# Kernel tuning notes

Hardware: AMD Instinct MI355X
Metric: run time of the kernel (lower is better)

## Reference

```python
import jax, jax.numpy as jnp
import numpy as np

B, T, I, H, O = 128, 500, 512, 1024, 11
BETA, THRESH, GAMMA, SPARSITY = 0.9, 1.0, 0.5, 0.05

@jax.custom_vjp
def spike(x):
    return (x > 0).astype(x.dtype)

def _spike_fwd(x):
    return (x > 0).astype(x.dtype), x

def _spike_bwd(x, g):
    # surrogate gradient: gamma / (1 + |x|)^2
    return (g * GAMMA / jnp.square(1.0 + jnp.abs(x)),)

spike.defvjp(_spike_fwd, _spike_bwd)


def setup_inputs() -> dict:
    key = jax.random.key(0)
    k0, k1, k2, k3, k4 = jax.random.split(key, 5)
    x = jax.random.normal(k0, (B, T, I), jnp.float32)
    # xavier-uniform-like init for W_in / W_out, orthogonal-ish (scaled normal) for W_rec
    lim_in = (6.0 / (I + H)) ** 0.5
    lim_out = (6.0 / (H + O)) ** 0.5
    W_in = jax.random.uniform(k1, (I, H), jnp.float32, -lim_in, lim_in)
    W_rec = jax.random.normal(k2, (H, H), jnp.float32) / jnp.sqrt(jnp.float32(H))
    W_out = jax.random.uniform(k3, (H, O), jnp.float32, -lim_out, lim_out)
    # fixed sparse connectivity mask: Bernoulli(sparsity), no self-connections
    mask = (jax.random.uniform(k4, (H, H)) < SPARSITY).astype(jnp.float32)
    mask = mask * (1.0 - jnp.eye(H, dtype=jnp.float32))
    W_rec = W_rec * mask  # reset_parameters() applies mask at init when mask is not learnable
    h_bias = jnp.zeros((H,), jnp.float32)
    b_out = jnp.zeros((O,), jnp.float32)
    return {"x": x, "W_in": W_in, "W_rec": W_rec, "W_out": W_out,
            "h_bias": h_bias, "b_out": b_out, "mask": mask}


def reference(x, W_in, W_rec, W_out, h_bias, b_out, mask):
    W_eff = W_rec * mask                                   # masked recurrent weights [H,H]
    drive = jnp.einsum('bti,ih->bth', x, W_in) + h_bias    # per-step input drive [B,T,H]
    drive_t = jnp.swapaxes(drive, 0, 1)                    # [T,B,H]

    def step(carry, d_t):
        v, s = carry
        v = BETA * v + d_t + s @ W_eff                     # LIF membrane update
        s_new = spike(v - THRESH)                          # surrogate threshold spike
        v = v - jax.lax.stop_gradient(s_new) * THRESH      # subtract reset (detached)
        out_t = s_new @ W_out + b_out                      # per-step readout [B,O]
        return (v, s_new), out_t

    init = (jnp.zeros((x.shape[0], W_eff.shape[0]), x.dtype),
            jnp.zeros((x.shape[0], W_eff.shape[0]), x.dtype))
    _, outs = jax.lax.scan(step, init, drive_t)            # outs: [T,B,O]
    return jnp.mean(outs, axis=0)                          # 'rate' readout -> [B,O]
```

## Files before the change

### kernel.cpp

```cpp
#include <hip/hip_runtime.h>
#include <cstdint>
#include <cstddef>

#define B_ 128
#define T_ 500
#define I_ 512
#define H_ 1024
#define O_ 11
#define BETA 0.9f
#define THRESH 1.0f
#define K2_ 1536

typedef __attribute__((ext_vector_type(4))) float f32x4;
typedef __attribute__((ext_vector_type(8))) short bf16x8;
typedef __attribute__((ext_vector_type(4))) unsigned int u32x4;

__device__ __forceinline__ unsigned short bf16_rne(float f) {
  unsigned int u = __float_as_uint(f);
  unsigned int r = u + 0x7FFFu + ((u >> 16) & 1u);
  return (unsigned short)(r >> 16);
}
__device__ __forceinline__ float bf16_to_f(unsigned short h) {
  return __uint_as_float(((unsigned int)h) << 16);
}

__global__ void k_csr(const float* __restrict__ W_rec, const float* __restrict__ mask,
                      unsigned int* __restrict__ csr, unsigned int* __restrict__ rowhi) {
  int r = blockIdx.x * 4 + (threadIdx.x >> 6);
  if (r > 1024) return;
  int lane = threadIdx.x & 63;
  unsigned cnt = 0;
  if (r < 1024) {
    const float* mrow = mask + (size_t)r * H_;
    const float* wrow = W_rec + (size_t)r * H_;
    for (int c = 0; c < 16; ++c) {
      float m = mrow[c * 64 + lane];
      bool nz = (m != 0.f);
      unsigned long long bb = __ballot(nz);
      unsigned pos = cnt + (unsigned)__popcll(bb & ((1ull << lane) - 1ull));
      if (nz) {
        float w = wrow[c * 64 + lane] * m;
        int wi = __float2int_rn(w * 8388608.f);
        wi = wi > 2097151 ? 2097151 : (wi < -2097151 ? -2097151 : wi);
        if (pos < 128u) csr[((size_t)r << 7) + pos] = (((unsigned)wi) << 10) | (unsigned)(c * 64 + lane);
      }
      cnt += (unsigned)__popcll(bb);
    }
  }
  for (unsigned p = (cnt > 128u ? 128u : cnt) + (unsigned)lane; p < 128u; p += 64u)
    csr[((size_t)r << 7) + p] = (p & 63u);
  if (lane == 0) rowhi[r] = (cnt > 64u) ? 1u : 0u;
}

__global__ void k_build_wt(const float* __restrict__ W_in, unsigned short* __restrict__ Wt) {
  int n = blockIdx.y;
  int k2 = blockIdx.x * 256 + threadIdx.x;
  int i = k2 / 3;
  int c = k2 - 3 * i;
  float w = W_in[i * H_ + n];
  unsigned short hi = bf16_rne(w);
  unsigned short v = (c == 2) ? bf16_rne(w - bf16_to_f(hi)) : hi;
  Wt[(size_t)n * K2_ + k2] = v;
}

__global__ void k_build_xs(const float* __restrict__ x, unsigned short* __restrict__ xs,
                           int t0, int Tc) {
  int id = blockIdx.x * 256 + threadIdx.x;
  int rr = id >> 6;
  int oct = id & 63;
  int b = rr / Tc, tt = rr % Tc;
  const float4 v0 = *(const float4*)&x[((size_t)(b * T_ + t0 + tt)) * I_ + oct * 8];
  const float4 v1 = *(const float4*)&x[((size_t)(b * T_ + t0 + tt)) * I_ + oct * 8 + 4];
  alignas(16) unsigned short o[24];
  float vv[8] = {v0.x, v0.y, v0.z, v0.w, v1.x, v1.y, v1.z, v1.w};
#pragma unroll
  for (int j = 0; j < 8; ++j) {
    unsigned short hi = bf16_rne(vv[j]);
    unsigned short lo = bf16_rne(vv[j] - bf16_to_f(hi));
    o[3 * j + 0] = hi; o[3 * j + 1] = lo; o[3 * j + 2] = hi;
  }
  unsigned short* dst = xs + (size_t)rr * K2_ + oct * 24;
  *(u32x4*)(dst + 0) = *(u32x4*)(o + 0);
  *(u32x4*)(dst + 8) = *(u32x4*)(o + 8);
  *(u32x4*)(dst + 16) = *(u32x4*)(o + 16);
}

#define LDA 72
__global__ __launch_bounds__(512, 1) void k_gemm(const unsigned short* __restrict__ xs,
                                                 const unsigned short* __restrict__ Wt,
                                                 float* __restrict__ drive) {
  __shared__ __align__(16) unsigned short As[128 * LDA];
  __shared__ __align__(16) unsigned short Bs[256 * LDA];
  int mt = blockIdx.x, nt = blockIdx.y;
  int tid = threadIdx.x;
  int lane = tid & 63, w = tid >> 6;
  int wr = w >> 2, wc = w & 3;
  f32x4 acc[4][4] = {};
  int arow = tid >> 2, aq = tid & 3;
  int brow = tid >> 1, bh = tid & 1;
  const unsigned short* xsrow = xs + (size_t)(mt * 128 + arow) * K2_ + aq * 16;
  const unsigned short* wtrow = Wt + (size_t)(nt * 256 + brow) * K2_ + bh * 32;
  for (int kt = 0; kt < K2_ / 64; ++kt) {
    u32x4 a0 = *(const u32x4*)(xsrow + kt * 64);
    u32x4 a1 = *(const u32x4*)(xsrow + kt * 64 + 8);
    u32x4 b0 = *(const u32x4*)(wtrow + kt * 64);
    u32x4 b1 = *(const u32x4*)(wtrow + kt * 64 + 8);
    u32x4 b2 = *(const u32x4*)(wtrow + kt * 64 + 16);
    u32x4 b3 = *(const u32x4*)(wtrow + kt * 64 + 24);
    __syncthreads();
    *(u32x4*)&As[arow * LDA + aq * 16] = a0;
    *(u32x4*)&As[arow * LDA + aq * 16 + 8] = a1;
    *(u32x4*)&Bs[brow * LDA + bh * 32] = b0;
    *(u32x4*)&Bs[brow * LDA + bh * 32 + 8] = b1;
    *(u32x4*)&Bs[brow * LDA + bh * 32 + 16] = b2;
    *(u32x4*)&Bs[brow * LDA + bh * 32 + 24] = b3;
    __syncthreads();
#pragma unroll
    for (int kk = 0; kk < 2; ++kk) {
      bf16x8 af[4], bf[4];
#pragma unroll
      for (int mi = 0; mi < 4; ++mi)
        af[mi] = *(const bf16x8*)&As[(wr * 64 + mi * 16 + (lane & 15)) * LDA + kk * 32 + (lane >> 4) * 8];
#pragma unroll
      for (int ni = 0; ni < 4; ++ni)
        bf[ni] = *(const bf16x8*)&Bs[(wc * 64 + ni * 16 + (lane & 15)) * LDA + kk * 32 + (lane >> 4) * 8];
#pragma unroll
      for (int mi = 0; mi < 4; ++mi)
#pragma unroll
        for (int ni = 0; ni < 4; ++ni)
          acc[mi][ni] = __builtin_amdgcn_mfma_f32_16x16x32_bf16(af[mi], bf[ni], acc[mi][ni], 0, 0, 0);
    }
  }
  int r0 = (lane >> 4) * 4, c0 = lane & 15;
#pragma unroll
  for (int mi = 0; mi < 4; ++mi) {
    int rowb = mt * 128 + wr * 64 + mi * 16 + r0;
#pragma unroll
    for (int ni = 0; ni < 4; ++ni) {
      int col = nt * 256 + wc * 64 + ni * 16 + c0;
#pragma unroll
      for (int r = 0; r < 4; ++r)
        drive[(size_t)(rowb + r) * H_ + col] = acc[mi][ni][r];
    }
  }
}

__device__ __forceinline__ void step_one(
    float dcur, int cur, int tid, int lane, unsigned wvu, unsigned myhi, float bias,
    const unsigned int* __restrict__ csr, int* accL, unsigned int* listL, unsigned int* fcL,
    float& v, float& s, float& cnt) {
  unsigned F = (unsigned)__builtin_amdgcn_readfirstlane((int)fcL[cur]);
  unsigned lo = (F * wvu) >> 4;
  unsigned hi = (F * (wvu + 1u)) >> 4;
  for (unsigned i0 = lo; i0 < hi; i0 += 8u) {
    unsigned idx = i0 + ((unsigned)lane & 7u);
    unsigned packed = listL[idx < hi ? idx : (hi - 1u)];
#define EDECL(n) unsigned e##n = (i0 + n##u < hi) ? (unsigned)__builtin_amdgcn_readlane((int)packed, n) : 1024u; \
                 unsigned ea##n = 0u, eb##n = 0u;
    EDECL(0) EDECL(1) EDECL(2) EDECL(3) EDECL(4) EDECL(5) EDECL(6) EDECL(7)
#undef EDECL
#define ELOAD(n) if (e##n != 1024u) { \
      const unsigned int* rp = csr + ((size_t)(e##n & 1023u) << 7); \
      ea##n = rp[lane]; \
      if (e##n & 4096u) eb##n = rp[64 + lane]; }
    ELOAD(0) ELOAD(1) ELOAD(2) ELOAD(3) ELOAD(4) ELOAD(5) ELOAD(6) ELOAD(7)
#undef ELOAD
#define EATOM(n) if (e##n != 1024u) { \
      atomicAdd(&accL[ea##n & 1023u], ((int)ea##n) >> 10); \
      if (e##n & 4096u) atomicAdd(&accL[eb##n & 1023u], ((int)eb##n) >> 10); }
    EATOM(0) EATOM(1) EATOM(2) EATOM(3) EATOM(4) EATOM(5) EATOM(6) EATOM(7)
#undef EATOM
  }
  __syncthreads();
  int ri = accL[tid];
  accL[tid] = 0;
  v = BETA * v + (dcur + bias) + (float)ri * 1.1920929e-7f;
  bool f = v > THRESH;
  v -= f ? THRESH : 0.f;
  cnt += f ? 1.f : 0.f;
  s = f ? 1.f : 0.f;
  unsigned long long bb = __ballot(f);
  unsigned n = (unsigned)__popcll(bb);
  unsigned pos = (unsigned)__popcll(bb & ((1ull << lane) - 1ull));
  unsigned wb = 0;
  if (lane == 0) wb = atomicAdd(&fcL[cur ^ 1], n);
  wb = (unsigned)__builtin_amdgcn_readfirstlane((int)wb);
  if (f) listL[wb + pos] = (unsigned)tid | myhi;
  if (tid == 0) fcL[cur] = 0;
  __syncthreads();
}

__global__ __launch_bounds__(1024, 1) void k_rsnn(
    const float* __restrict__ drive, const unsigned int* __restrict__ csr,
    const unsigned int* __restrict__ rowhi,
    const float* __restrict__ h_bias, const float* __restrict__ W_out,
    const float* __restrict__ b_out,
    float* __restrict__ state_v, float* __restrict__ state_s, float* __restrict__ state_c,
    float* __restrict__ out, int t0, int Tc, int last) {
  __shared__ int accL[H_];
  __shared__ unsigned int listL[H_];
  __shared__ unsigned int fcL[2];
  __shared__ float red[H_];
  __shared__ float part[352];
  int tid = threadIdx.x;
  int b = blockIdx.x;
  int lane = tid & 63;
  unsigned wvu = (unsigned)__builtin_amdgcn_readfirstlane(tid >> 6);
  float bias = h_bias[tid];
  unsigned myhi = rowhi[tid] << 12;
  float v, s, cnt;
  if (t0 == 0) { v = 0.f; s = 0.f; cnt = 0.f; }
  else { v = state_v[b * H_ + tid]; s = state_s[b * H_ + tid]; cnt = state_c[b * H_ + tid]; }
  accL[tid] = 0;
  if (tid < 2) fcL[tid] = 0;
  __syncthreads();
  {
    bool f0 = s > 0.f;
    unsigned long long bb = __ballot(f0);
    unsigned n = (unsigned)__popcll(bb);
    unsigned pos = (unsigned)__popcll(bb & ((1ull << lane) - 1ull));
    unsigned wb = 0;
    if (lane == 0) wb = atomicAdd(&fcL[0], n);
    wb = (unsigned)__builtin_amdgcn_readfirstlane((int)wb);
    if (f0) listL[wb + pos] = (unsigned)tid | myhi;
  }
  __syncthreads();
  const float* dptr = drive + (size_t)b * Tc * H_ + tid;
  for (int t8 = 0; t8 < Tc; t8 += 8) {
    float dd0 = (t8 + 0 < Tc) ? dptr[(size_t)(t8 + 0) * H_] : 0.f;
    float dd1 = (t8 + 1 < Tc) ? dptr[(size_t)(t8 + 1) * H_] : 0.f;
    float dd2 = (t8 + 2 < Tc) ? dptr[(size_t)(t8 + 2) * H_] : 0.f;
    float dd3 = (t8 + 3 < Tc) ? dptr[(size_t)(t8 + 3) * H_] : 0.f;
    float dd4 = (t8 + 4 < Tc) ? dptr[(size_t)(t8 + 4) * H_] : 0.f;
    float dd5 = (t8 + 5 < Tc) ? dptr[(size_t)(t8 + 5) * H_] : 0.f;
    float dd6 = (t8 + 6 < Tc) ? dptr[(size_t)(t8 + 6) * H_] : 0.f;
    float dd7 = (t8 + 7 < Tc) ? dptr[(size_t)(t8 + 7) * H_] : 0.f;
#define STEP(s_) if (t8 + s_ < Tc) \
    step_one(dd##s_, (s_ & 1), tid, lane, wvu, myhi, bias, csr, accL, listL, fcL, v, s, cnt);
    STEP(0) STEP(1) STEP(2) STEP(3) STEP(4) STEP(5) STEP(6) STEP(7)
#undef STEP
  }
  if (!last) {
    state_v[b * H_ + tid] = v; state_s[b * H_ + tid] = s; state_c[b * H_ + tid] = cnt;
  } else {
    red[tid] = cnt;
    __syncthreads();
    if (tid < 352) {
      int o = tid >> 5, seg = tid & 31;
      float p = 0.f;
      for (int j = 0; j < 32; ++j) {
        int hh = seg * 32 + j;
        p += red[hh] * W_out[hh * O_ + o];
      }
      part[tid] = p;
    }
    __syncthreads();
    if (tid < O_) {
      float sum = 0.f;
      for (int g = 0; g < 32; ++g) sum += part[(tid << 5) + g];
      out[b * O_ + tid] = b_out[tid] + sum * (1.0f / (float)T_);
    }
  }
}

extern "C" void kernel_launch(void* const* d_in, const int* in_sizes, int n_in,
                              void* d_out, int out_size, void* d_ws, size_t ws_size,
                              hipStream_t stream) {
  (void)in_sizes; (void)n_in; (void)out_size;
  const float* x = (const float*)d_in[0];
  const float* W_in = (const float*)d_in[1];
  const float* W_rec = (const float*)d_in[2];
  const float* W_out = (const float*)d_in[3];
  const float* h_bias = (const float*)d_in[4];
  const float* b_out = (const float*)d_in[5];
  const float* mask = (const float*)d_in[6];
  float* out = (float*)d_out;

  char* ws = (char*)d_ws;
  size_t off = 0;
  auto alloc = [&](size_t bytes) {
    void* p = ws + off;
    off = (off + bytes + 255) & ~(size_t)255;
    return p;
  };
  unsigned short* Wt = (unsigned short*)alloc((size_t)H_ * K2_ * 2);
  unsigned int* csr = (unsigned int*)alloc((size_t)(H_ + 1) * 128 * 4);
  unsigned int* rowhi = (unsigned int*)alloc((size_t)(H_ + 1) * 4);
  float* st_v = (float*)alloc((size_t)B_ * H_ * 4);
  float* st_s = (float*)alloc((size_t)B_ * H_ * 4);
  float* st_c = (float*)alloc((size_t)B_ * H_ * 4);
  size_t fixed = off;

  size_t per_t = (size_t)128 * K2_ * 2 + (size_t)128 * 1024 * 4;
  int Tc = 1;
  if (ws_size > fixed + per_t) Tc = (int)((ws_size - fixed) / per_t);
  if (Tc > T_) Tc = T_;
  if (Tc < 1) Tc = 1;
  unsigned short* xs = (unsigned short*)alloc((size_t)128 * Tc * K2_ * 2);
  float* drive = (float*)alloc((size_t)128 * Tc * 1024 * 4);

  k_csr<<<dim3(257), dim3(256), 0, stream>>>(W_rec, mask, csr, rowhi);
  k_build_wt<<<dim3(6, 1024), dim3(256), 0, stream>>>(W_in, Wt);

  for (int t0 = 0; t0 < T_; t0 += Tc) {
    int tc = (Tc < T_ - t0) ? Tc : (T_ - t0);
    k_build_xs<<<dim3(32 * tc), dim3(256), 0, stream>>>(x, xs, t0, tc);
    k_gemm<<<dim3(tc, 4), dim3(512), 0, stream>>>(xs, Wt, drive);
    k_rsnn<<<dim3(128), dim3(1024), 0, stream>>>(drive, csr, rowhi, h_bias, W_out, b_out,
                                                 st_v, st_s, st_c, out, t0, tc,
                                                 (t0 + tc >= T_) ? 1 : 0);
  }
}
```

Baseline: 1.048 ms.

## Fuse x bf16 split into GEMM A-tile load and reorder K layout

Drops the separate k_build_xs kernel and its bf16x3 staging buffer. The GEMM now reads fp32 x directly and converts each A tile to hi or lo bf16 inside the load loop. K2 is reorganised from interleaved triples into three contiguous 512-wide segments (hi, lo, hi), and W_in is built to match. The GEMM grid is also swizzled so groups of 8 m-tiles share the same n-tile for better L2 reuse. This removes a full write and read of the expanded x array, but x is now reread three times and converted in the GEMM load path, which adds ALU work there.

```diff
diff --git a/kernel.cpp b/kernel.cpp
--- a/kernel.cpp
+++ b/kernel.cpp
@@ -27,25 +27,22 @@
 __global__ void k_csr(const float* __restrict__ W_rec, const float* __restrict__ mask,
                       unsigned int* __restrict__ csr, unsigned int* __restrict__ rowhi) {
   int r = blockIdx.x * 4 + (threadIdx.x >> 6);
-  if (r > 1024) return;
   int lane = threadIdx.x & 63;
   unsigned cnt = 0;
-  if (r < 1024) {
-    const float* mrow = mask + (size_t)r * H_;
-    const float* wrow = W_rec + (size_t)r * H_;
-    for (int c = 0; c < 16; ++c) {
-      float m = mrow[c * 64 + lane];
-      bool nz = (m != 0.f);
-      unsigned long long bb = __ballot(nz);
-      unsigned pos = cnt + (unsigned)__popcll(bb & ((1ull << lane) - 1ull));
-      if (nz) {
-        float w = wrow[c * 64 + lane] * m;
-        int wi = __float2int_rn(w * 8388608.f);
-        wi = wi > 2097151 ? 2097151 : (wi < -2097151 ? -2097151 : wi);
-        if (pos < 128u) csr[((size_t)r << 7) + pos] = (((unsigned)wi) << 10) | (unsigned)(c * 64 + lane);
-      }
-      cnt += (unsigned)__popcll(bb);
-    }
+  const float* mrow = mask + (size_t)r * H_;
+  const float* wrow = W_rec + (size_t)r * H_;
+  for (int c = 0; c < 16; ++c) {
+    float m = mrow[c * 64 + lane];
+    bool nz = (m != 0.f);
+    unsigned long long bb = __ballot(nz);
+    unsigned pos = cnt + (unsigned)__popcll(bb & ((1ull << lane) - 1ull));
+    if (nz) {
+      float w = wrow[c * 64 + lane] * m;
+      int wi = __float2int_rn(w * 8388608.f);
+      wi = wi > 2097151 ? 2097151 : (wi < -2097151 ? -2097151 : wi);
+      if (pos < 128u) csr[((size_t)r << 7) + pos] = (((unsigned)wi) << 10) | (unsigned)(c * 64 + lane);
+    }
+    cnt += (unsigned)__popcll(bb);
   }
   for (unsigned p = (cnt > 128u ? 128u : cnt) + (unsigned)lane; p < 128u; p += 64u)
     csr[((size_t)r << 7) + p] = (p & 63u);
@@ -55,61 +52,58 @@
 __global__ void k_build_wt(const float* __restrict__ W_in, unsigned short* __restrict__ Wt) {
   int n = blockIdx.y;
   int k2 = blockIdx.x * 256 + threadIdx.x;
-  int i = k2 / 3;
-  int c = k2 - 3 * i;
+  int i = k2 & 511;
+  int c = k2 >> 9;
   float w = W_in[i * H_ + n];
   unsigned short hi = bf16_rne(w);
   unsigned short v = (c == 2) ? bf16_rne(w - bf16_to_f(hi)) : hi;
   Wt[(size_t)n * K2_ + k2] = v;
 }
 
-__global__ void k_build_xs(const float* __restrict__ x, unsigned short* __restrict__ xs,
-                           int t0, int Tc) {
-  int id = blockIdx.x * 256 + threadIdx.x;
-  int rr = id >> 6;
-  int oct = id & 63;
-  int b = rr / Tc, tt = rr % Tc;
-  const float4 v0 = *(const float4*)&x[((size_t)(b * T_ + t0 + tt)) * I_ + oct * 8];
-  const float4 v1 = *(const float4*)&x[((size_t)(b * T_ + t0 + tt)) * I_ + oct * 8 + 4];
-  alignas(16) unsigned short o[24];
-  float vv[8] = {v0.x, v0.y, v0.z, v0.w, v1.x, v1.y, v1.z, v1.w};
-#pragma unroll
-  for (int j = 0; j < 8; ++j) {
-    unsigned short hi = bf16_rne(vv[j]);
-    unsigned short lo = bf16_rne(vv[j] - bf16_to_f(hi));
-    o[3 * j + 0] = hi; o[3 * j + 1] = lo; o[3 * j + 2] = hi;
-  }
-  unsigned short* dst = xs + (size_t)rr * K2_ + oct * 24;
-  *(u32x4*)(dst + 0) = *(u32x4*)(o + 0);
-  *(u32x4*)(dst + 8) = *(u32x4*)(o + 8);
-  *(u32x4*)(dst + 16) = *(u32x4*)(o + 16);
-}
-
 #define LDA 72
-__global__ __launch_bounds__(512, 1) void k_gemm(const unsigned short* __restrict__ xs,
+__global__ __launch_bounds__(512, 1) void k_gemm(const float* __restrict__ x,
                                                  const unsigned short* __restrict__ Wt,
-                                                 float* __restrict__ drive) {
+                                                 float* __restrict__ drive,
+                                                 int t0, int Tc) {
   __shared__ __align__(16) unsigned short As[128 * LDA];
   __shared__ __align__(16) unsigned short Bs[256 * LDA];
-  int mt = blockIdx.x, nt = blockIdx.y;
+  int id = blockIdx.x;
+  int mt = (id >> 5) * 8 + (id & 7);
+  int nt = (id >> 3) & 3;
+  if (mt >= Tc) return;
   int tid = threadIdx.x;
   int lane = tid & 63, w = tid >> 6;
   int wr = w >> 2, wc = w & 3;
   f32x4 acc[4][4] = {};
   int arow = tid >> 2, aq = tid & 3;
   int brow = tid >> 1, bh = tid & 1;
-  const unsigned short* xsrow = xs + (size_t)(mt * 128 + arow) * K2_ + aq * 16;
+  int rr = mt * 128 + arow;
+  int bb = rr / Tc, tt = rr - bb * Tc;
+  const float* xrow = x + ((size_t)(bb * T_ + t0 + tt)) * I_ + aq * 16;
   const unsigned short* wtrow = Wt + (size_t)(nt * 256 + brow) * K2_ + bh * 32;
   for (int kt = 0; kt < K2_ / 64; ++kt) {
-    u32x4 a0 = *(const u32x4*)(xsrow + kt * 64);
-    u32x4 a1 = *(const u32x4*)(xsrow + kt * 64 + 8);
+    int creg = kt >> 3;
+    int i0 = (kt & 7) * 64;
+    const float* ap = xrow + i0;
+    float4 a0 = *(const float4*)(ap);
+    float4 a1 = *(const float4*)(ap + 4);
+    float4 a2 = *(const float4*)(ap + 8);
+    float4 a3 = *(const float4*)(ap + 12);
     u32x4 b0 = *(const u32x4*)(wtrow + kt * 64);
     u32x4 b1 = *(const u32x4*)(wtrow + kt * 64 + 8);
     u32x4 b2 = *(const u32x4*)(wtrow + kt * 64 + 16);
     u32x4 b3 = *(const u32x4*)(wtrow + kt * 64 + 24);
+    alignas(16) unsigned short o[16];
+    float vv[16] = {a0.x, a0.y, a0.z, a0.w, a1.x, a1.y, a1.z, a1.w,
+                    a2.x, a2.y, a2.z, a2.w, a3.x, a3.y, a3.z, a3.w};
+#pragma unroll
+    for (int j = 0; j < 16; ++j) {
+      unsigned short hi = bf16_rne(vv[j]);
+      o[j] = (creg == 1) ? bf16_rne(vv[j] - bf16_to_f(hi)) : hi;
+    }
     __syncthreads();
-    *(u32x4*)&As[arow * LDA + aq * 16] = a0;
-    *(u32x4*)&As[arow * LDA + aq * 16 + 8] = a1;
+    *(u32x4*)&As[arow * LDA + aq * 16] = *(u32x4*)o;
+    *(u32x4*)&As[arow * LDA + aq * 16 + 8] = *(u32x4*)(o + 8);
     *(u32x4*)&Bs[brow * LDA + bh * 32] = b0;
     *(u32x4*)&Bs[brow * LDA + bh * 32 + 8] = b1;
     *(u32x4*)&Bs[brow * LDA + bh * 32 + 16] = b2;
@@ -284,28 +278,27 @@
     return p;
   };
   unsigned short* Wt = (unsigned short*)alloc((size_t)H_ * K2_ * 2);
-  unsigned int* csr = (unsigned int*)alloc((size_t)(H_ + 1) * 128 * 4);
-  unsigned int* rowhi = (unsigned int*)alloc((size_t)(H_ + 1) * 4);
+  unsigned int* csr = (unsigned int*)alloc((size_t)H_ * 128 * 4);
+  unsigned int* rowhi = (unsigned int*)alloc((size_t)H_ * 4);
   float* st_v = (float*)alloc((size_t)B_ * H_ * 4);
   float* st_s = (float*)alloc((size_t)B_ * H_ * 4);
   float* st_c = (float*)alloc((size_t)B_ * H_ * 4);
   size_t fixed = off;
 
-  size_t per_t = (size_t)128 * K2_ * 2 + (size_t)128 * 1024 * 4;
+  size_t per_t = (size_t)128 * 1024 * 4;
   int Tc = 1;
   if (ws_size > fixed + per_t) Tc = (int)((ws_size - fixed) / per_t);
   if (Tc > T_) Tc = T_;
   if (Tc < 1) Tc = 1;
-  unsigned short* xs = (unsigned short*)alloc((size_t)128 * Tc * K2_ * 2);
   float* drive = (float*)alloc((size_t)128 * Tc * 1024 * 4);
 
-  k_csr<<<dim3(257), dim3(256), 0, stream>>>(W_rec, mask, csr, rowhi);
+  k_csr<<<dim3(256), dim3(256), 0, stream>>>(W_rec, mask, csr, rowhi);
   k_build_wt<<<dim3(6, 1024), dim3(256), 0, stream>>>(W_in, Wt);
 
   for (int t0 = 0; t0 < T_; t0 += Tc) {
     int tc = (Tc < T_ - t0) ? Tc : (T_ - t0);
-    k_build_xs<<<dim3(32 * tc), dim3(256), 0, stream>>>(x, xs, t0, tc);
-    k_gemm<<<dim3(tc, 4), dim3(512), 0, stream>>>(xs, Wt, drive);
+    int groups = (tc + 7) / 8;
+    k_gemm<<<dim3(groups * 32), dim3(512), 0, stream>>>(x, Wt, drive, t0, tc);
     k_rsnn<<<dim3(128), dim3(1024), 0, stream>>>(drive, csr, rowhi, h_bias, W_out, b_out,
                                                  st_v, st_s, st_c, out, t0, tc,
                                                  (t0 + tc >= T_) ? 1 : 0);
```

After: 999.0 us. 1.05x faster.
